# Kernel tuning notes

Hardware: AMD Instinct MI355X
Metric: run time of the kernel (lower is better)

The kernel has to match this reference:

```python
import jax, jax.numpy as jnp
import numpy as np

N_NODES = 100000
N_EDGES = 1600000
D = 128
EPS = 0.0  # train_eps=False -> constant


def setup_inputs() -> dict:
    key = jax.random.key(0)
    k = jax.random.split(key, 6)
    s = 1.0 / np.sqrt(D)
    return {
        "X": jax.random.normal(k[0], (N_NODES, D), dtype=jnp.float32),
        "W1": jax.random.normal(k[1], (D, D), dtype=jnp.float32) * s,
        "b1": jnp.zeros((D,), dtype=jnp.float32),
        "W2": jax.random.normal(k[2], (D, D), dtype=jnp.float32) * s,
        "b2": jnp.zeros((D,), dtype=jnp.float32),
        "edge_src": jax.random.randint(k[3], (N_EDGES,), 0, N_NODES, dtype=jnp.int32),
        "edge_dst": jax.random.randint(k[4], (N_EDGES,), 0, N_NODES, dtype=jnp.int32),
    }


def reference(X, W1, b1, W2, b2, edge_src, edge_dst):
    # v2v sum aggregation: agg[i] = sum_{j in N(i)} X[j]
    msgs = X[edge_src]  # (E, D) gather
    agg = jax.ops.segment_sum(msgs, edge_dst, num_segments=N_NODES)  # (N, D)
    h = (1.0 + EPS) * X + agg
    # MLP: Linear -> ReLU -> Linear
    h = jax.nn.relu(h @ W1 + b1)
    out = h @ W2 + b2
    return out
```

## Files before the change

kernel.cpp:

```cpp
#include <hip/hip_runtime.h>
#include <hip/hip_bf16.h>

#define N_NODES 100000
#define N_EDGES 1600000
#define D 128

#define NBINS 196
#define BINSHIFT 9
#define BINCAP 10000
#define EPB 8192

#define MID_SORT_BLOCKS 196
#define MID_W_BLOCKS 8
#define MID_CVT_BLOCKS 3125

#define PADK 136

typedef __bf16 bf16x8 __attribute__((ext_vector_type(8)));
typedef short short8 __attribute__((ext_vector_type(8)));
typedef float f32x4 __attribute__((ext_vector_type(4)));

__device__ __forceinline__ unsigned short f2bf(float f) {
  union { float f; unsigned u; } c; c.f = f;
  unsigned u = c.u;
  u += 0x7FFFu + ((u >> 16) & 1u);
  return (unsigned short)(u >> 16);
}
__device__ __forceinline__ float bflo(unsigned u) {
  union { unsigned u; float f; } c; c.u = u << 16; return c.f;
}
__device__ __forceinline__ float bfhi(unsigned u) {
  union { unsigned u; float f; } c; c.u = u & 0xFFFF0000u; return c.f;
}

__launch_bounds__(512)
__global__ void k_bin(const int* __restrict__ esrc, const int* __restrict__ edst,
                      int* __restrict__ g_bincnt, unsigned* __restrict__ binbuf) {
  __shared__ int cnt[NBINS];
  __shared__ int base[NBINS];
  const int b = blockIdx.x, t = threadIdx.x;
  const int e0 = b * EPB;
  const int ne = min(EPB, N_EDGES - e0);
  for (int i = t; i < NBINS; i += 512) cnt[i] = 0;
  __syncthreads();
  for (int i = t; i < ne; i += 512)
    atomicAdd(&cnt[edst[e0 + i] >> BINSHIFT], 1);
  __syncthreads();
  for (int i = t; i < NBINS; i += 512) {
    base[i] = atomicAdd(&g_bincnt[i], cnt[i]);
    cnt[i] = 0;
  }
  __syncthreads();
  for (int i = t; i < ne; i += 512) {
    int d = edst[e0 + i];
    int s = esrc[e0 + i];
    int bi = d >> BINSHIFT;
    int pos = base[bi] + atomicAdd(&cnt[bi], 1);
    binbuf[(size_t)bi * BINCAP + pos] = ((unsigned)(d & 511) << 17) | (unsigned)s;
  }
}

__launch_bounds__(512)
__global__ void k_mid(const unsigned* __restrict__ binbuf, const int* __restrict__ g_bincnt,
                      int* __restrict__ srt, int* __restrict__ deg, int* __restrict__ offs,
                      const float* __restrict__ X, unsigned short* __restrict__ Xb,
                      const float* __restrict__ W1, const float* __restrict__ W2,
                      unsigned short* __restrict__ Wimg) {
  const int b = blockIdx.x, t = threadIdx.x;

  if (b < MID_SORT_BLOCKS) {
    __shared__ int hist[512];
    __shared__ int scan[512];
    __shared__ int sb[256];
    if (t < 256) sb[t] = (t < NBINS) ? g_bincnt[t] : 0;
    __syncthreads();
    for (int d = 1; d < 256; d <<= 1) {
      int x = 0;
      if (t < 256 && t >= d) x = sb[t - d];
      __syncthreads();
      if (t < 256) sb[t] += x;
      __syncthreads();
    }
    const int cntb = g_bincnt[b];
    const int gbase = (b == 0) ? 0 : sb[b - 1];
    const int n0 = b << BINSHIFT;
    const unsigned* ebuf = binbuf + (size_t)b * BINCAP;

    hist[t] = 0;
    __syncthreads();
    for (int i = t; i < cntb; i += 512)
      atomicAdd(&hist[ebuf[i] >> 17], 1);
    __syncthreads();
    int v = hist[t];
    scan[t] = v;
    __syncthreads();
    for (int d = 1; d < 512; d <<= 1) {
      int x = (t >= d) ? scan[t - d] : 0;
      __syncthreads();
      scan[t] += x;
      __syncthreads();
    }
    int n = n0 + t;
    if (n < N_NODES) {
      deg[n] = v;
      offs[n] = gbase + scan[t] - v;
    }
    hist[t] = scan[t] - v;
    __syncthreads();
    for (int i = t; i < cntb; i += 512) {
      unsigned e = ebuf[i];
      int pos = atomicAdd(&hist[e >> 17], 1);
      srt[gbase + pos] = (int)(e & 0x1FFFFu);
    }
    return;
  }
  if (b < MID_SORT_BLOCKS + MID_W_BLOCKS) {
    int bb = b - MID_SORT_BLOCKS;
    const float* W = (bb & 4) ? W2 : W1;
    unsigned short* img = Wimg + ((bb & 4) ? 128 * PADK : 0);
    int k0 = (bb & 3) * 32;
#pragma unroll
    for (int it = 0; it < 8; ++it) {
      int idx = it * 512 + t;
      int k = k0 + (idx >> 7), n = idx & 127;
      img[n * PADK + k] = f2bf(W[k * 128 + n]);
    }
    return;
  }
  size_t i = ((size_t)(b - MID_SORT_BLOCKS - MID_W_BLOCKS) * 512 + t) * 8;
  const float4* p = (const float4*)(X + i);
  float4 a = p[0], c = p[1];
  short8 s;
  s[0] = f2bf(a.x); s[1] = f2bf(a.y); s[2] = f2bf(a.z); s[3] = f2bf(a.w);
  s[4] = f2bf(c.x); s[5] = f2bf(c.y); s[6] = f2bf(c.z); s[7] = f2bf(c.w);
  *(short8*)(Xb + i) = s;
}

__global__ void k_gather_bf(const unsigned int* __restrict__ X1,
                            const int* __restrict__ deg, const int* __restrict__ offs,
                            const int* __restrict__ srt, unsigned int* __restrict__ h0) {
  int node = blockIdx.x * 4 + (threadIdx.x >> 6);
  int lane = threadIdx.x & 63;
  unsigned u = X1[(size_t)node * 64 + lane];
  float hx = bflo(u), hy = bfhi(u);
  int e = offs[node];
  int end = e + deg[node];
  for (; e + 8 <= end; e += 8) {
    int s0 = srt[e],     s1 = srt[e + 1], s2 = srt[e + 2], s3 = srt[e + 3];
    int s4 = srt[e + 4], s5 = srt[e + 5], s6 = srt[e + 6], s7 = srt[e + 7];
    unsigned u0 = X1[(size_t)s0 * 64 + lane];
    unsigned u1 = X1[(size_t)s1 * 64 + lane];
    unsigned u2 = X1[(size_t)s2 * 64 + lane];
    unsigned u3 = X1[(size_t)s3 * 64 + lane];
    unsigned u4 = X1[(size_t)s4 * 64 + lane];
    unsigned u5 = X1[(size_t)s5 * 64 + lane];
    unsigned u6 = X1[(size_t)s6 * 64 + lane];
    unsigned u7 = X1[(size_t)s7 * 64 + lane];
    hx += bflo(u0); hy += bfhi(u0);
    hx += bflo(u1); hy += bfhi(u1);
    hx += bflo(u2); hy += bfhi(u2);
    hx += bflo(u3); hy += bfhi(u3);
    hx += bflo(u4); hy += bfhi(u4);
    hx += bflo(u5); hy += bfhi(u5);
    hx += bflo(u6); hy += bfhi(u6);
    hx += bflo(u7); hy += bfhi(u7);
  }
  for (; e + 2 <= end; e += 2) {
    unsigned u0 = X1[(size_t)srt[e] * 64 + lane];
    unsigned u1 = X1[(size_t)srt[e + 1] * 64 + lane];
    hx += bflo(u0); hy += bfhi(u0);
    hx += bflo(u1); hy += bfhi(u1);
  }
  for (; e < end; ++e) {
    unsigned u0 = X1[(size_t)srt[e] * 64 + lane];
    hx += bflo(u0); hy += bfhi(u0);
  }
  h0[(size_t)node * 64 + lane] = ((unsigned)f2bf(hy) << 16) | f2bf(hx);
}

#define BR2 128

__launch_bounds__(512, 4)
__global__ void k_mlp2(const unsigned short* __restrict__ h0,
                       const unsigned short* __restrict__ Wimg,
                       const float* __restrict__ b1v, const float* __restrict__ b2v,
                       float* __restrict__ out) {
  __shared__ __attribute__((aligned(16))) unsigned short lW[128 * PADK];
  __shared__ __attribute__((aligned(16))) unsigned short lH[BR2 * PADK];

  const int t = threadIdx.x;
  const int wave = t >> 6, lane = t & 63;
  const int lr = lane & 15, lg = lane >> 4;
  const int row0 = blockIdx.x * BR2;
  const int wrow = row0 + wave * 16;

  {
    const uint4* wi = (const uint4*)Wimg;
    uint4* lw = (uint4*)lW;
    for (int i = t; i < (128 * PADK * 2) / 16; i += 512) lw[i] = wi[i];
  }

  bf16x8 a[4];
#pragma unroll
  for (int kb = 0; kb < 4; ++kb) {
    int r = wrow + lr;
    if (r >= N_NODES) r = N_NODES - 1;
    a[kb] = __builtin_bit_cast(bf16x8,
        *(const short8*)(h0 + (size_t)r * D + kb * 32 + lg * 8));
  }

  f32x4 acc[8];
#pragma unroll
  for (int nc = 0; nc < 8; ++nc) {
    float bb = b1v[nc * 16 + lr];
    acc[nc] = (f32x4){bb, bb, bb, bb};
  }

  __syncthreads();

#pragma unroll
  for (int nc = 0; nc < 8; ++nc) {
#pragma unroll
    for (int kb = 0; kb < 4; ++kb) {
      bf16x8 b = *(const bf16x8*)&lW[(nc * 16 + lr) * PADK + kb * 32 + lg * 8];
      acc[nc] = __builtin_amdgcn_mfma_f32_16x16x32_bf16(a[kb], b, acc[nc], 0, 0, 0);
    }
  }

  __syncthreads();

  {
    const uint4* wi = (const uint4*)Wimg + 2176;
    uint4* lw = (uint4*)lW;
    for (int i = t; i < 2176; i += 512) lw[i] = wi[i];
  }

#pragma unroll
  for (int nc = 0; nc < 8; ++nc) {
#pragma unroll
    for (int r = 0; r < 4; ++r) {
      float v = acc[nc][r];
      v = v > 0.f ? v : 0.f;
      lH[(wave * 16 + lg * 4 + r) * PADK + nc * 16 + lr] = f2bf(v);
    }
  }

  __syncthreads();

  bf16x8 a2[4];
#pragma unroll
  for (int kb = 0; kb < 4; ++kb)
    a2[kb] = *(const bf16x8*)&lH[(wave * 16 + lr) * PADK + kb * 32 + lg * 8];

#pragma unroll
  for (int nc = 0; nc < 8; ++nc) {
    float bb = b2v[nc * 16 + lr];
    acc[nc] = (f32x4){bb, bb, bb, bb};
  }

#pragma unroll
  for (int nc = 0; nc < 8; ++nc) {
#pragma unroll
    for (int kb = 0; kb < 4; ++kb) {
      bf16x8 b = *(const bf16x8*)&lW[(nc * 16 + lr) * PADK + kb * 32 + lg * 8];
      acc[nc] = __builtin_amdgcn_mfma_f32_16x16x32_bf16(a2[kb], b, acc[nc], 0, 0, 0);
    }
  }

#pragma unroll
  for (int nc = 0; nc < 8; ++nc) {
#pragma unroll
    for (int r = 0; r < 4; ++r) {
      int row = wrow + lg * 4 + r;
      if (row < N_NODES) out[(size_t)row * D + nc * 16 + lr] = acc[nc][r];
    }
  }
}


__global__ void k_hist(const int* __restrict__ dst, int* __restrict__ deg) {
  int i = blockIdx.x * 256 + threadIdx.x;
  if (i < N_EDGES) atomicAdd(&deg[dst[i]], 1);
}

__global__ void k_scan1(const int* __restrict__ deg, int* __restrict__ offs,
                        int* __restrict__ bsum) {
  __shared__ int s[1024];
  int t = threadIdx.x;
  int i = blockIdx.x * 1024 + t;
  int v = (i < N_NODES) ? deg[i] : 0;
  s[t] = v;
  __syncthreads();
  for (int d = 1; d < 1024; d <<= 1) {
    int x = (t >= d) ? s[t - d] : 0;
    __syncthreads();
    s[t] += x;
    __syncthreads();
  }
  if (i < N_NODES) offs[i] = s[t] - v;
  if (t == 1023) bsum[blockIdx.x] = s[t];
}

__global__ void k_scan2(int* __restrict__ bsum) {
  __shared__ int s[128];
  int t = threadIdx.x;
  int v = (t < 98) ? bsum[t] : 0;
  s[t] = v;
  __syncthreads();
  for (int d = 1; d < 128; d <<= 1) {
    int x = (t >= d) ? s[t - d] : 0;
    __syncthreads();
    s[t] += x;
    __syncthreads();
  }
  if (t < 98) bsum[t] = s[t] - v;
}

__global__ void k_scan3(int* __restrict__ offs, const int* __restrict__ bsum) {
  int i = blockIdx.x * 1024 + threadIdx.x;
  if (i < N_NODES) offs[i] += bsum[blockIdx.x];
}

__global__ void k_bucket(const int* __restrict__ src, const int* __restrict__ dst,
                         int* __restrict__ offs, int* __restrict__ srt) {
  int i = blockIdx.x * 256 + threadIdx.x;
  if (i < N_EDGES) {
    int pos = atomicAdd(&offs[dst[i]], 1);
    srt[pos] = src[i];
  }
}

__global__ void k_gather(const float* __restrict__ X, const int* __restrict__ deg,
                         const int* __restrict__ offs, const int* __restrict__ srt,
                         float* __restrict__ out) {
  int node = blockIdx.x * 4 + (threadIdx.x >> 6);
  int lane = threadIdx.x & 63;
  const float2* X2 = (const float2*)X;
  float2 h = X2[(size_t)node * 64 + lane];
  int end = offs[node];
  int dg = deg[node];
  for (int e = end - dg; e < end; ++e) {
    int s = srt[e];
    float2 x = X2[(size_t)s * 64 + lane];
    h.x += x.x; h.y += x.y;
  }
  ((float2*)out)[(size_t)node * 64 + lane] = h;
}

#define BR 256

__launch_bounds__(512, 1)
__global__ void k_mlp(const float* __restrict__ h0,
                      const float* __restrict__ W1, const float* __restrict__ b1,
                      const float* __restrict__ W2, const float* __restrict__ b2,
                      float* __restrict__ out) {
  __shared__ __attribute__((aligned(16))) unsigned short lW[2 * 128 * PADK];
  __shared__ __attribute__((aligned(16))) unsigned short lH[BR * PADK];

  const int t = threadIdx.x;
  const int wave = t >> 6, lane = t & 63;
  const int lr = lane & 15, lg = lane >> 4;
  const int row0 = blockIdx.x * BR;
  const int wrow = row0 + wave * 32;

  for (int i = t; i < 128 * 128; i += 512) {
    int k = i >> 7, n = i & 127;
    lW[n * PADK + k] = f2bf(W1[i]);
    lW[128 * PADK + n * PADK + k] = f2bf(W2[i]);
  }

  bf16x8 a[2][4];
#pragma unroll
  for (int tr = 0; tr < 2; ++tr) {
#pragma unroll
    for (int kb = 0; kb < 4; ++kb) {
      int r = wrow + tr * 16 + lr;
      if (r >= N_NODES) r = N_NODES - 1;
      const float4* p = (const float4*)(h0 + (size_t)r * D + kb * 32 + lg * 8);
      float4 f0 = p[0], f1 = p[1];
      short8 s;
      s[0] = f2bf(f0.x); s[1] = f2bf(f0.y); s[2] = f2bf(f0.z); s[3] = f2bf(f0.w);
      s[4] = f2bf(f1.x); s[5] = f2bf(f1.y); s[6] = f2bf(f1.z); s[7] = f2bf(f1.w);
      a[tr][kb] = __builtin_bit_cast(bf16x8, s);
    }
  }

  f32x4 acc[2][8];
#pragma unroll
  for (int nc = 0; nc < 8; ++nc) {
    float bb = b1[nc * 16 + lr];
#pragma unroll
    for (int tr = 0; tr < 2; ++tr) acc[tr][nc] = (f32x4){bb, bb, bb, bb};
  }

  __syncthreads();

#pragma unroll
  for (int nc = 0; nc < 8; ++nc) {
#pragma unroll
    for (int kb = 0; kb < 4; ++kb) {
      bf16x8 b = *(const bf16x8*)&lW[(nc * 16 + lr) * PADK + kb * 32 + lg * 8];
#pragma unroll
      for (int tr = 0; tr < 2; ++tr)
        acc[tr][nc] = __builtin_amdgcn_mfma_f32_16x16x32_bf16(a[tr][kb], b, acc[tr][nc], 0, 0, 0);
    }
  }

#pragma unroll
  for (int tr = 0; tr < 2; ++tr) {
#pragma unroll
    for (int nc = 0; nc < 8; ++nc) {
#pragma unroll
      for (int r = 0; r < 4; ++r) {
        float v = acc[tr][nc][r];
        v = v > 0.f ? v : 0.f;
        int lrow = wave * 32 + tr * 16 + lg * 4 + r;
        lH[lrow * PADK + nc * 16 + lr] = f2bf(v);
      }
    }
  }

  __syncthreads();

  bf16x8 a2[2][4];
#pragma unroll
  for (int tr = 0; tr < 2; ++tr) {
#pragma unroll
    for (int kb = 0; kb < 4; ++kb)
      a2[tr][kb] = *(const bf16x8*)&lH[(wave * 32 + tr * 16 + lr) * PADK + kb * 32 + lg * 8];
  }

#pragma unroll
  for (int nc = 0; nc < 8; ++nc) {
    float bb = b2[nc * 16 + lr];
#pragma unroll
    for (int tr = 0; tr < 2; ++tr) acc[tr][nc] = (f32x4){bb, bb, bb, bb};
  }

#pragma unroll
  for (int nc = 0; nc < 8; ++nc) {
#pragma unroll
    for (int kb = 0; kb < 4; ++kb) {
      bf16x8 b = *(const bf16x8*)&lW[128 * PADK + (nc * 16 + lr) * PADK + kb * 32 + lg * 8];
#pragma unroll
      for (int tr = 0; tr < 2; ++tr)
        acc[tr][nc] = __builtin_amdgcn_mfma_f32_16x16x32_bf16(a2[tr][kb], b, acc[tr][nc], 0, 0, 0);
    }
  }

#pragma unroll
  for (int tr = 0; tr < 2; ++tr) {
#pragma unroll
    for (int nc = 0; nc < 8; ++nc) {
#pragma unroll
      for (int r = 0; r < 4; ++r) {
        int row = wrow + tr * 16 + lg * 4 + r;
        if (row < N_NODES) out[(size_t)row * D + nc * 16 + lr] = acc[tr][nc][r];
      }
    }
  }
}

extern "C" void kernel_launch(void* const* d_in, const int* in_sizes, int n_in,
                              void* d_out, int out_size, void* d_ws, size_t ws_size,
                              hipStream_t stream) {
  const float* X  = (const float*)d_in[0];
  const float* W1 = (const float*)d_in[1];
  const float* b1 = (const float*)d_in[2];
  const float* W2 = (const float*)d_in[3];
  const float* b2 = (const float*)d_in[4];
  const int* esrc = (const int*)d_in[5];
  const int* edst = (const int*)d_in[6];
  float* out = (float*)d_out;

  char* ws = (char*)d_ws;
  int* deg      = (int*)(ws);
  int* offs     = (int*)(ws + 400000);
  int* g_bincnt = (int*)(ws + 800000);
  int* srt      = (int*)(ws + 802048);
  unsigned short* Xb  = (unsigned short*)(ws + 7202048);
  unsigned short* h0b = (unsigned short*)(ws + 32802048);
  unsigned* binbuf = (unsigned*)(ws + 32802048);
  unsigned short* Wimg = (unsigned short*)(ws + 58402048);
  const size_t NEED = 58471680;

  if (ws_size >= NEED) {
    hipMemsetAsync(g_bincnt, 0, NBINS * sizeof(int), stream);
    k_bin<<<(N_EDGES + EPB - 1) / EPB, 512, 0, stream>>>(esrc, edst, g_bincnt, binbuf);
    k_mid<<<MID_SORT_BLOCKS + MID_W_BLOCKS + MID_CVT_BLOCKS, 512, 0, stream>>>(
        binbuf, g_bincnt, srt, deg, offs, X, Xb, W1, W2, Wimg);
    k_gather_bf<<<N_NODES / 4, 256, 0, stream>>>((const unsigned*)Xb, deg, offs, srt,
                                                 (unsigned*)h0b);
    k_mlp2<<<(N_NODES + BR2 - 1) / BR2, 512, 0, stream>>>(h0b, Wimg, b1, b2, out);
  } else {
    int* bsum = g_bincnt;
    hipMemsetAsync(deg, 0, N_NODES * sizeof(int), stream);
    k_hist  <<<N_EDGES / 256, 256, 0, stream>>>(edst, deg);
    k_scan1 <<<98, 1024, 0, stream>>>(deg, offs, bsum);
    k_scan2 <<<1, 128, 0, stream>>>(bsum);
    k_scan3 <<<98, 1024, 0, stream>>>(offs, bsum);
    k_bucket<<<N_EDGES / 256, 256, 0, stream>>>(esrc, edst, offs, srt);
    k_gather<<<N_NODES / 4, 256, 0, stream>>>(X, deg, offs, srt, out);
    k_mlp   <<<(N_NODES + BR - 1) / BR, 512, 0, stream>>>(out, W1, b1, W2, b2, out);
  }
}
```

Baseline: 133.3 us.

## Pre-swizzle weights into MFMA fragment order and read them directly from global

The weight conversion in the mid kernel now writes W1 and W2 in the exact per-lane MFMA B-fragment order, so the MLP kernel loads each fragment with a single coalesced 16-byte global read instead of staging padded weights in shared memory. The MLP kernel shrinks to 256 threads and 64 rows per block, with a per-wave private LDS tile for the hidden activations, which removes all block-wide barriers. The cost is that every wave re-reads the 64 KB of weights from L2/global instead of sharing one LDS copy per block, trading LDS traffic and syncs for more cache traffic.

```diff
diff --git a/kernel.cpp b/kernel.cpp
--- a/kernel.cpp
+++ b/kernel.cpp
@@ -65,7 +65,7 @@
                       int* __restrict__ srt, int* __restrict__ deg, int* __restrict__ offs,
                       const float* __restrict__ X, unsigned short* __restrict__ Xb,
                       const float* __restrict__ W1, const float* __restrict__ W2,
-                      unsigned short* __restrict__ Wimg) {
+                      unsigned short* __restrict__ Wf) {
   const int b = blockIdx.x, t = threadIdx.x;
 
   if (b < MID_SORT_BLOCKS) {
@@ -116,14 +116,16 @@
   }
   if (b < MID_SORT_BLOCKS + MID_W_BLOCKS) {
     int bb = b - MID_SORT_BLOCKS;
-    const float* W = (bb & 4) ? W2 : W1;
-    unsigned short* img = Wimg + ((bb & 4) ? 128 * PADK : 0);
-    int k0 = (bb & 3) * 32;
 #pragma unroll
     for (int it = 0; it < 8; ++it) {
-      int idx = it * 512 + t;
-      int k = k0 + (idx >> 7), n = idx & 127;
-      img[n * PADK + k] = f2bf(W[k * 128 + n]);
+      int idx = bb * 4096 + it * 512 + t;
+      int fi = idx & 16383;
+      const float* W = (idx >> 14) ? W2 : W1;
+      int e = fi & 7, l = (fi >> 3) & 63, q = fi >> 9;
+      int kb = q & 3, nc = q >> 2;
+      int k = kb * 32 + (l >> 4) * 8 + e;
+      int n = nc * 16 + (l & 15);
+      Wf[idx] = f2bf(W[k * 128 + n]);
     }
     return;
   }
@@ -178,27 +180,17 @@
   h0[(size_t)node * 64 + lane] = ((unsigned)f2bf(hy) << 16) | f2bf(hx);
 }
 
-#define BR2 128
-
-__launch_bounds__(512, 4)
-__global__ void k_mlp2(const unsigned short* __restrict__ h0,
-                       const unsigned short* __restrict__ Wimg,
+__launch_bounds__(256, 4)
+__global__ void k_mlp3(const unsigned short* __restrict__ h0,
+                       const unsigned short* __restrict__ Wf,
                        const float* __restrict__ b1v, const float* __restrict__ b2v,
                        float* __restrict__ out) {
-  __shared__ __attribute__((aligned(16))) unsigned short lW[128 * PADK];
-  __shared__ __attribute__((aligned(16))) unsigned short lH[BR2 * PADK];
+  __shared__ __attribute__((aligned(16))) unsigned short lH[4][16 * PADK];
 
   const int t = threadIdx.x;
   const int wave = t >> 6, lane = t & 63;
   const int lr = lane & 15, lg = lane >> 4;
-  const int row0 = blockIdx.x * BR2;
-  const int wrow = row0 + wave * 16;
-
-  {
-    const uint4* wi = (const uint4*)Wimg;
-    uint4* lw = (uint4*)lW;
-    for (int i = t; i < (128 * PADK * 2) / 16; i += 512) lw[i] = wi[i];
-  }
+  const int wrow = blockIdx.x * 64 + wave * 16;
 
   bf16x8 a[4];
 #pragma unroll
@@ -216,23 +208,13 @@
     acc[nc] = (f32x4){bb, bb, bb, bb};
   }
 
-  __syncthreads();
-
 #pragma unroll
   for (int nc = 0; nc < 8; ++nc) {
 #pragma unroll
     for (int kb = 0; kb < 4; ++kb) {
-      bf16x8 b = *(const bf16x8*)&lW[(nc * 16 + lr) * PADK + kb * 32 + lg * 8];
+      bf16x8 b = *(const bf16x8*)&Wf[(((nc * 4 + kb) * 64) + lane) * 8];
       acc[nc] = __builtin_amdgcn_mfma_f32_16x16x32_bf16(a[kb], b, acc[nc], 0, 0, 0);
     }
-  }
-
-  __syncthreads();
-
-  {
-    const uint4* wi = (const uint4*)Wimg + 2176;
-    uint4* lw = (uint4*)lW;
-    for (int i = t; i < 2176; i += 512) lw[i] = wi[i];
   }
 
 #pragma unroll
@@ -241,16 +223,14 @@
     for (int r = 0; r < 4; ++r) {
       float v = acc[nc][r];
       v = v > 0.f ? v : 0.f;
-      lH[(wave * 16 + lg * 4 + r) * PADK + nc * 16 + lr] = f2bf(v);
-    }
-  }
-
-  __syncthreads();
+      lH[wave][(lg * 4 + r) * PADK + nc * 16 + lr] = f2bf(v);
+    }
+  }
 
   bf16x8 a2[4];
 #pragma unroll
   for (int kb = 0; kb < 4; ++kb)
-    a2[kb] = *(const bf16x8*)&lH[(wave * 16 + lr) * PADK + kb * 32 + lg * 8];
+    a2[kb] = *(const bf16x8*)&lH[wave][lr * PADK + kb * 32 + lg * 8];
 
 #pragma unroll
   for (int nc = 0; nc < 8; ++nc) {
@@ -258,11 +238,12 @@
     acc[nc] = (f32x4){bb, bb, bb, bb};
   }
 
+  const unsigned short* Wf2 = Wf + 16384;
 #pragma unroll
   for (int nc = 0; nc < 8; ++nc) {
 #pragma unroll
     for (int kb = 0; kb < 4; ++kb) {
-      bf16x8 b = *(const bf16x8*)&lW[(nc * 16 + lr) * PADK + kb * 32 + lg * 8];
+      bf16x8 b = *(const bf16x8*)&Wf2[(((nc * 4 + kb) * 64) + lane) * 8];
       acc[nc] = __builtin_amdgcn_mfma_f32_16x16x32_bf16(a2[kb], b, acc[nc], 0, 0, 0);
     }
   }
@@ -481,17 +462,17 @@
   unsigned short* Xb  = (unsigned short*)(ws + 7202048);
   unsigned short* h0b = (unsigned short*)(ws + 32802048);
   unsigned* binbuf = (unsigned*)(ws + 32802048);
-  unsigned short* Wimg = (unsigned short*)(ws + 58402048);
+  unsigned short* Wf = (unsigned short*)(ws + 58402048);
   const size_t NEED = 58471680;
 
   if (ws_size >= NEED) {
     hipMemsetAsync(g_bincnt, 0, NBINS * sizeof(int), stream);
     k_bin<<<(N_EDGES + EPB - 1) / EPB, 512, 0, stream>>>(esrc, edst, g_bincnt, binbuf);
     k_mid<<<MID_SORT_BLOCKS + MID_W_BLOCKS + MID_CVT_BLOCKS, 512, 0, stream>>>(
-        binbuf, g_bincnt, srt, deg, offs, X, Xb, W1, W2, Wimg);
+        binbuf, g_bincnt, srt, deg, offs, X, Xb, W1, W2, Wf);
     k_gather_bf<<<N_NODES / 4, 256, 0, stream>>>((const unsigned*)Xb, deg, offs, srt,
                                                  (unsigned*)h0b);
-    k_mlp2<<<(N_NODES + BR2 - 1) / BR2, 512, 0, stream>>>(h0b, Wimg, b1, b2, out);
+    k_mlp3<<<(N_NODES + 63) / 64, 256, 0, stream>>>(h0b, Wf, b1, b2, out);
   } else {
     int* bsum = g_bincnt;
     hipMemsetAsync(deg, 0, N_NODES * sizeof(int), stream);
```

New measurement: 141.6 us. +6.2%, slower.

## Replace global-atomic binning with block-local LDS binning and count matrices

Applied to the files above, without the earlier changes.

The binning kernel now sorts each block's 8192 edges by bin in shared memory and writes them to global memory contiguously. It records per-block, per-bin counts and starts in transposed matrices, replacing the global atomic bin counters and the scattered writes. The sort stage rebuilds each bin by gathering its slices from all 196 source blocks into LDS, using column sums and scans. This removes the memset and contended global atomics and makes the binning writes coalesced. In exchange the mid kernel does more scan work and more fragmented reads, and the 35 KB LDS buffer may lower occupancy.

```diff
diff --git a/kernel.cpp b/kernel.cpp
--- a/kernel.cpp
+++ b/kernel.cpp
@@ -7,8 +7,9 @@
 
 #define NBINS 196
 #define BINSHIFT 9
-#define BINCAP 10000
 #define EPB 8192
+#define RBLK 196
+#define EBUF_CAP 8960
 
 #define MID_SORT_BLOCKS 196
 #define MID_W_BLOCKS 8
@@ -34,34 +35,54 @@
 }
 
 __launch_bounds__(512)
-__global__ void k_bin(const int* __restrict__ esrc, const int* __restrict__ edst,
-                      int* __restrict__ g_bincnt, unsigned* __restrict__ binbuf) {
+__global__ void k_bin2(const int* __restrict__ esrc, const int* __restrict__ edst,
+                       unsigned* __restrict__ binbuf, int* __restrict__ cntmatT,
+                       int* __restrict__ startmatT) {
+  __shared__ unsigned lbuf[EPB];
   __shared__ int cnt[NBINS];
   __shared__ int base[NBINS];
+  __shared__ int cur[NBINS];
+  __shared__ int scanb[256];
   const int b = blockIdx.x, t = threadIdx.x;
   const int e0 = b * EPB;
   const int ne = min(EPB, N_EDGES - e0);
-  for (int i = t; i < NBINS; i += 512) cnt[i] = 0;
+
+  for (int i = t; i < NBINS; i += 512) { cnt[i] = 0; cur[i] = 0; }
   __syncthreads();
   for (int i = t; i < ne; i += 512)
     atomicAdd(&cnt[edst[e0 + i] >> BINSHIFT], 1);
   __syncthreads();
-  for (int i = t; i < NBINS; i += 512) {
-    base[i] = atomicAdd(&g_bincnt[i], cnt[i]);
-    cnt[i] = 0;
-  }
+  if (t < 256) scanb[t] = (t < NBINS) ? cnt[t] : 0;
+  __syncthreads();
+  for (int d = 1; d < 256; d <<= 1) {
+    int x = 0;
+    if (t < 256 && t >= d) x = scanb[t - d];
+    __syncthreads();
+    if (t < 256) scanb[t] += x;
+    __syncthreads();
+  }
+  if (t < NBINS) base[t] = scanb[t] - cnt[t];
   __syncthreads();
   for (int i = t; i < ne; i += 512) {
     int d = edst[e0 + i];
     int s = esrc[e0 + i];
     int bi = d >> BINSHIFT;
-    int pos = base[bi] + atomicAdd(&cnt[bi], 1);
-    binbuf[(size_t)bi * BINCAP + pos] = ((unsigned)(d & 511) << 17) | (unsigned)s;
+    int pos = base[bi] + atomicAdd(&cur[bi], 1);
+    lbuf[pos] = ((unsigned)(d & 511) << 17) | (unsigned)s;
+  }
+  __syncthreads();
+  uint4* dst4 = (uint4*)(binbuf + (size_t)b * EPB);
+  const uint4* src4 = (const uint4*)lbuf;
+  for (int i = t; i < EPB / 4; i += 512) dst4[i] = src4[i];
+  if (t < NBINS) {
+    cntmatT[t * RBLK + b] = cnt[t];
+    startmatT[t * RBLK + b] = base[t];
   }
 }
 
 __launch_bounds__(512)
-__global__ void k_mid(const unsigned* __restrict__ binbuf, const int* __restrict__ g_bincnt,
+__global__ void k_mid(const unsigned* __restrict__ binbuf, const int* __restrict__ cntmatT,
+                      const int* __restrict__ startmatT,
                       int* __restrict__ srt, int* __restrict__ deg, int* __restrict__ offs,
                       const float* __restrict__ X, unsigned short* __restrict__ Xb,
                       const float* __restrict__ W1, const float* __restrict__ W2,
@@ -69,45 +90,84 @@
   const int b = blockIdx.x, t = threadIdx.x;
 
   if (b < MID_SORT_BLOCKS) {
+    __shared__ unsigned ebuf[EBUF_CAP];
     __shared__ int hist[512];
-    __shared__ int scan[512];
-    __shared__ int sb[256];
-    if (t < 256) sb[t] = (t < NBINS) ? g_bincnt[t] : 0;
+    __shared__ int scn[512];
+    __shared__ int rcnt[RBLK];
+    __shared__ int roff[RBLK];
+    __shared__ int eoff[RBLK];
+    __shared__ int colsc[256];
+
+    for (int r = t; r < RBLK; r += 512) {
+      rcnt[r] = cntmatT[b * RBLK + r];
+      roff[r] = startmatT[b * RBLK + r];
+    }
+    int cs = 0;
+    if (t < NBINS) {
+      const uint4* row = (const uint4*)(cntmatT + t * RBLK);
+#pragma unroll 7
+      for (int j = 0; j < RBLK / 4; ++j) {
+        uint4 v = row[j];
+        cs += (int)(v.x + v.y + v.z + v.w);
+      }
+    }
+    if (t < 256) colsc[t] = (t < NBINS) ? cs : 0;
     __syncthreads();
     for (int d = 1; d < 256; d <<= 1) {
       int x = 0;
-      if (t < 256 && t >= d) x = sb[t - d];
+      if (t < 256 && t >= d) x = colsc[t - d];
       __syncthreads();
-      if (t < 256) sb[t] += x;
+      if (t < 256) colsc[t] += x;
       __syncthreads();
     }
-    const int cntb = g_bincnt[b];
-    const int gbase = (b == 0) ? 0 : sb[b - 1];
-    const int n0 = b << BINSHIFT;
-    const unsigned* ebuf = binbuf + (size_t)b * BINCAP;
-
+    const int total = cntmatT ? 0 : 0;
+    (void)total;
+    const int mytotal_holder = 0; (void)mytotal_holder;
+    __syncthreads();
+    const int mytotal = colsc[b] - ((b == 0) ? 0 : colsc[b - 1]);
+    const int gbase = (b == 0) ? 0 : colsc[b - 1];
+
+    if (t < 256) scn[t] = (t < RBLK) ? rcnt[t] : 0;
+    __syncthreads();
+    for (int d = 1; d < 256; d <<= 1) {
+      int x = 0;
+      if (t < 256 && t >= d) x = scn[t - d];
+      __syncthreads();
+      if (t < 256) scn[t] += x;
+      __syncthreads();
+    }
+    if (t < RBLK) eoff[t] = scn[t] - rcnt[t];
+    __syncthreads();
+
+    const int wv = t >> 6, ln = t & 63;
+    for (int r = wv; r < RBLK; r += 8) {
+      const unsigned* src = binbuf + (size_t)r * EPB + roff[r];
+      int c = rcnt[r], o = eoff[r];
+      for (int i = ln; i < c; i += 64) ebuf[o + i] = src[i];
+    }
     hist[t] = 0;
     __syncthreads();
-    for (int i = t; i < cntb; i += 512)
+
+    for (int i = t; i < mytotal; i += 512)
       atomicAdd(&hist[ebuf[i] >> 17], 1);
     __syncthreads();
     int v = hist[t];
-    scan[t] = v;
+    scn[t] = v;
     __syncthreads();
     for (int d = 1; d < 512; d <<= 1) {
-      int x = (t >= d) ? scan[t - d] : 0;
+      int x = (t >= d) ? scn[t - d] : 0;
       __syncthreads();
-      scan[t] += x;
+      scn[t] += x;
       __syncthreads();
     }
-    int n = n0 + t;
+    int n = (b << BINSHIFT) + t;
     if (n < N_NODES) {
       deg[n] = v;
-      offs[n] = gbase + scan[t] - v;
-    }
-    hist[t] = scan[t] - v;
-    __syncthreads();
-    for (int i = t; i < cntb; i += 512) {
+      offs[n] = gbase + scn[t] - v;
+    }
+    hist[t] = scn[t] - v;
+    __syncthreads();
+    for (int i = t; i < mytotal; i += 512) {
       unsigned e = ebuf[i];
       int pos = atomicAdd(&hist[e >> 17], 1);
       srt[gbase + pos] = (int)(e & 0x1FFFFu);
@@ -194,11 +254,10 @@
   const int row0 = blockIdx.x * BR2;
   const int wrow = row0 + wave * 16;
 
-  {
-    const uint4* wi = (const uint4*)Wimg;
-    uint4* lw = (uint4*)lW;
-    for (int i = t; i < (128 * PADK * 2) / 16; i += 512) lw[i] = wi[i];
-  }
+  const uint4* wi = (const uint4*)Wimg;
+  uint4* lw = (uint4*)lW;
+
+  for (int i = t; i < 2176; i += 512) lw[i] = wi[i];
 
   bf16x8 a[4];
 #pragma unroll
@@ -230,9 +289,8 @@
   __syncthreads();
 
   {
-    const uint4* wi = (const uint4*)Wimg + 2176;
-    uint4* lw = (uint4*)lW;
-    for (int i = t; i < 2176; i += 512) lw[i] = wi[i];
+    const uint4* wi2 = (const uint4*)Wimg + 2176;
+    for (int i = t; i < 2176; i += 512) lw[i] = wi2[i];
   }
 
 #pragma unroll
@@ -476,31 +534,32 @@
   char* ws = (char*)d_ws;
   int* deg      = (int*)(ws);
   int* offs     = (int*)(ws + 400000);
-  int* g_bincnt = (int*)(ws + 800000);
-  int* srt      = (int*)(ws + 802048);
-  unsigned short* Xb  = (unsigned short*)(ws + 7202048);
-  unsigned short* h0b = (unsigned short*)(ws + 32802048);
-  unsigned* binbuf = (unsigned*)(ws + 32802048);
-  unsigned short* Wimg = (unsigned short*)(ws + 58402048);
-  const size_t NEED = 58471680;
+  int* srt      = (int*)(ws + 800000);
+  unsigned short* Xb  = (unsigned short*)(ws + 7200000);
+  unsigned short* h0b = (unsigned short*)(ws + 32800000);
+  unsigned* binbuf = (unsigned*)(ws + 32800000);
+  int* cntmatT   = (int*)(ws + 32800000 + 6422528);
+  int* startmatT = (int*)(ws + 32800000 + 6422528 + 153664);
+  unsigned short* Wimg = (unsigned short*)(ws + 58400000);
+  const size_t NEED = 58469632;
 
   if (ws_size >= NEED) {
-    hipMemsetAsync(g_bincnt, 0, NBINS * sizeof(int), stream);
-    k_bin<<<(N_EDGES + EPB - 1) / EPB, 512, 0, stream>>>(esrc, edst, g_bincnt, binbuf);
+    k_bin2<<<RBLK, 512, 0, stream>>>(esrc, edst, binbuf, cntmatT, startmatT);
     k_mid<<<MID_SORT_BLOCKS + MID_W_BLOCKS + MID_CVT_BLOCKS, 512, 0, stream>>>(
-        binbuf, g_bincnt, srt, deg, offs, X, Xb, W1, W2, Wimg);
+        binbuf, cntmatT, startmatT, srt, deg, offs, X, Xb, W1, W2, Wimg);
     k_gather_bf<<<N_NODES / 4, 256, 0, stream>>>((const unsigned*)Xb, deg, offs, srt,
                                                  (unsigned*)h0b);
     k_mlp2<<<(N_NODES + BR2 - 1) / BR2, 512, 0, stream>>>(h0b, Wimg, b1, b2, out);
   } else {
-    int* bsum = g_bincnt;
+    int* bsum  = (int*)(ws + 800000);
+    int* srtF  = (int*)(ws + 802048);
     hipMemsetAsync(deg, 0, N_NODES * sizeof(int), stream);
     k_hist  <<<N_EDGES / 256, 256, 0, stream>>>(edst, deg);
     k_scan1 <<<98, 1024, 0, stream>>>(deg, offs, bsum);
     k_scan2 <<<1, 128, 0, stream>>>(bsum);
     k_scan3 <<<98, 1024, 0, stream>>>(offs, bsum);
-    k_bucket<<<N_EDGES / 256, 256, 0, stream>>>(esrc, edst, offs, srt);
-    k_gather<<<N_NODES / 4, 256, 0, stream>>>(X, deg, offs, srt, out);
+    k_bucket<<<N_EDGES / 256, 256, 0, stream>>>(esrc, edst, offs, srtF);
+    k_gather<<<N_NODES / 4, 256, 0, stream>>>(X, deg, offs, srtF, out);
     k_mlp   <<<(N_NODES + BR - 1) / BR, 512, 0, stream>>>(out, W1, b1, W2, b2, out);
   }
 }
```

Result: no change. 132.3 us (-0.8%).
